# Optimization experiments

Hardware: AMD Instinct MI355X
Metric: run time of the kernel (lower is better)

The kernel has to match this reference:

```python
import jax, jax.numpy as jnp
import numpy as np

B, S, H = 32, 4096, 512

def setup_inputs() -> dict:
    key = jax.random.key(0)
    k1, k2, k3 = jax.random.split(key, 3)
    h_t = jax.random.normal(k1, (B, H), dtype=jnp.float32)
    context = jax.random.normal(k2, (B, S, H), dtype=jnp.float32)
    W = jax.random.normal(k3, (H, H), dtype=jnp.float32) * (1.0 / np.sqrt(H))
    pos = 7  # current cyclic-buffer write index (self.it % seq_len)
    return {"h_t": h_t, "context": context, "W": W, "pos": pos}

def reference(h_t, context, W, pos):
    # Luong 'general' attention: score[b,s] = h_t[b] . (W @ context[b,s])
    scores = jnp.einsum('bh,hk,bsk->bs', h_t, W, context)  # [B,S]
    attn = jax.nn.softmax(scores, axis=-1)                  # softmax over buffer slots
    # weighted sum over the context buffer -> [B,H]
    cntx = jnp.einsum('bs,bsh->bh', attn, context)
    # cyclic buffer write: add_vector(h_t) at slot pos (detached in original)
    new_buffer = context.at[:, pos % context.shape[1], :].set(h_t)
    return cntx, new_buffer
```

## Files before the change

### kernel.cpp

```cpp
#include <hip/hip_runtime.h>
#include <math.h>

constexpr int B = 32, S = 4096, H = 512;
constexpr int BDIM = 256;
constexpr int MAX_SPLIT = 64;

typedef float f4 __attribute__((ext_vector_type(4)));

__global__ __launch_bounds__(BDIM) void u_kernel(const float* __restrict__ h_t,
                                                 const float* __restrict__ W,
                                                 float* __restrict__ u) {
    const int b = blockIdx.y;
    const int k = blockIdx.x * BDIM + threadIdx.x;
    __shared__ float hs[H];
    for (int i = threadIdx.x; i < H; i += BDIM) hs[i] = h_t[b * H + i];
    __syncthreads();
    float acc = 0.f;
#pragma unroll 8
    for (int h = 0; h < H; ++h) acc = fmaf(hs[h], W[h * H + k], acc);
    u[b * H + k] = acc;
}

__global__ __launch_bounds__(BDIM) void flash_kernel(const float* __restrict__ ctx,
                                                     const float* __restrict__ h_t,
                                                     const float* __restrict__ u,
                                                     const int* __restrict__ posp,
                                                     float* __restrict__ newbuf,
                                                     float* __restrict__ pacc,
                                                     float* __restrict__ pml,
                                                     int nsplit) {
    const int b     = blockIdx.y;
    const int split = blockIdx.x;
    const int w     = threadIdx.x >> 6;
    const int lane  = threadIdx.x & 63;
    const int rpb   = S / nsplit;
    const int s0    = split * rpb;
    int pos = posp[0] % S; if (pos < 0) pos += S;

    const f4* ub = (const f4*)(u + (size_t)b * H);
    const f4 u0 = ub[lane], u1 = ub[64 + lane];
    const f4* hb = (const f4*)(h_t + (size_t)b * H);
    const f4 h0 = hb[lane], h1 = hb[64 + lane];

    float m = -INFINITY, l = 0.f;
    f4 a0 = {0.f, 0.f, 0.f, 0.f}, a1 = {0.f, 0.f, 0.f, 0.f};

#pragma unroll 2
    for (int s = s0 + w; s < s0 + rpb; s += 4) {
        const f4* crow = (const f4*)(ctx + ((size_t)b * S + s) * H);
        const f4 c0 = __builtin_nontemporal_load(crow + lane);
        const f4 c1 = __builtin_nontemporal_load(crow + 64 + lane);

        f4* orow = (f4*)(newbuf + ((size_t)b * S + s) * H);
        const f4 o0 = (s == pos) ? h0 : c0;
        const f4 o1 = (s == pos) ? h1 : c1;
        __builtin_nontemporal_store(o0, orow + lane);
        __builtin_nontemporal_store(o1, orow + 64 + lane);

        float d = c0.x * u0.x + c0.y * u0.y + c0.z * u0.z + c0.w * u0.w
                + c1.x * u1.x + c1.y * u1.y + c1.z * u1.z + c1.w * u1.w;
#pragma unroll
        for (int off = 32; off >= 1; off >>= 1) d += __shfl_xor(d, off);

        const float nm = fmaxf(m, d);
        const float sc = __expf(m - nm);
        const float p  = __expf(d - nm);
        a0 = a0 * sc + p * c0;
        a1 = a1 * sc + p * c1;
        l = l * sc + p;
        m = nm;
    }

    __shared__ float lacc[4][H];
    __shared__ float lml[4][2];
    f4* dst = (f4*)&lacc[w][0];
    dst[lane] = a0; dst[64 + lane] = a1;
    if (lane == 0) { lml[w][0] = m; lml[w][1] = l; }
    __syncthreads();

    const float m0 = lml[0][0], m1 = lml[1][0], m2 = lml[2][0], m3 = lml[3][0];
    const float M  = fmaxf(fmaxf(m0, m1), fmaxf(m2, m3));
    const float e0 = __expf(m0 - M), e1 = __expf(m1 - M);
    const float e2 = __expf(m2 - M), e3 = __expf(m3 - M);

    const int t    = threadIdx.x;
    const int pidx = b * nsplit + split;
    const float ca = e0 * lacc[0][t]       + e1 * lacc[1][t]
                   + e2 * lacc[2][t]       + e3 * lacc[3][t];
    const float cb = e0 * lacc[0][256 + t] + e1 * lacc[1][256 + t]
                   + e2 * lacc[2][256 + t] + e3 * lacc[3][256 + t];
    pacc[(size_t)pidx * H + t]       = ca;
    pacc[(size_t)pidx * H + 256 + t] = cb;
    if (t == 0) {
        const float L = e0 * lml[0][1] + e1 * lml[1][1]
                      + e2 * lml[2][1] + e3 * lml[3][1];
        pml[2 * pidx] = M; pml[2 * pidx + 1] = L;
    }
}

__global__ __launch_bounds__(BDIM) void combine_kernel(const float* __restrict__ pacc,
                                                       const float* __restrict__ pml,
                                                       float* __restrict__ cntx,
                                                       int nsplit) {
    const int b    = blockIdx.x;
    const int half = blockIdx.y;
    const int t    = threadIdx.x;
    const int col  = half * 256 + t;

    __shared__ float lm[MAX_SPLIT], ll[MAX_SPLIT];
    for (int p = t; p < nsplit; p += BDIM) {
        lm[p] = pml[2 * (b * nsplit + p)];
        ll[p] = pml[2 * (b * nsplit + p) + 1];
    }
    __syncthreads();

    float M = -INFINITY;
    for (int p = 0; p < nsplit; ++p) M = fmaxf(M, lm[p]);

    float acc = 0.f, L = 0.f;
    for (int p = 0; p < nsplit; ++p) {
        const float e = __expf(lm[p] - M);
        L   = fmaf(e, ll[p], L);
        acc = fmaf(e, pacc[(size_t)(b * nsplit + p) * H + col], acc);
    }
    cntx[b * H + col] = acc / L;
}

extern "C" void kernel_launch(void* const* d_in, const int* in_sizes, int n_in,
                              void* d_out, int out_size, void* d_ws, size_t ws_size,
                              hipStream_t stream) {
    const float* h_t = (const float*)d_in[0];
    const float* ctx = (const float*)d_in[1];
    const float* W   = (const float*)d_in[2];
    const int*   pos = (const int*)d_in[3];

    float* out    = (float*)d_out;
    float* cntx   = out;
    float* newbuf = out + (size_t)B * H;

    char*  ws = (char*)d_ws;
    float* u  = (float*)ws;
    const size_t u_bytes = (size_t)B * H * sizeof(float);

    int nsplit = MAX_SPLIT;
    while (nsplit > 1) {
        const size_t need = u_bytes
                          + (size_t)B * nsplit * H * sizeof(float)
                          + (size_t)B * nsplit * 2 * sizeof(float);
        if (need <= ws_size) break;
        nsplit >>= 1;
    }
    float* pacc = (float*)(ws + u_bytes);
    float* pml  = pacc + (size_t)B * nsplit * H;

    u_kernel<<<dim3(H / BDIM, B), BDIM, 0, stream>>>(h_t, W, u);
    flash_kernel<<<dim3(nsplit, B), BDIM, 0, stream>>>(ctx, h_t, u, pos, newbuf,
                                                       pacc, pml, nsplit);
    combine_kernel<<<dim3(B, 2), BDIM, 0, stream>>>(pacc, pml, cntx, nsplit);
}
```

Measured before the change: 131.3 us.

## Fuse combine into flash kernel via last-block atomic, use exp2 with lazy rescale

Removes the separate combine kernel launch: each split block increments a per-batch atomic counter, and the last block to finish merges all partial results. The counter is reset inside u_kernel. Scores are pre-scaled by log2(e) so exp2f can be used, and the running-max rescale is skipped unless the score exceeds the current max by a threshold, which cuts per-row exponentials. The u_kernel also gets four independent accumulators, and the flash loop unroll goes from 2 to 4. The costs are threadfence/atomic synchronisation and a serial tail combine done by one block per batch.

```diff
diff --git a/kernel.cpp b/kernel.cpp
--- a/kernel.cpp
+++ b/kernel.cpp
@@ -4,21 +4,30 @@
 constexpr int B = 32, S = 4096, H = 512;
 constexpr int BDIM = 256;
 constexpr int MAX_SPLIT = 64;
+constexpr float LOG2E = 1.44269504088896340736f;
+constexpr float DEFER_THR = 11.5415603f;
 
 typedef float f4 __attribute__((ext_vector_type(4)));
 
 __global__ __launch_bounds__(BDIM) void u_kernel(const float* __restrict__ h_t,
                                                  const float* __restrict__ W,
-                                                 float* __restrict__ u) {
+                                                 float* __restrict__ u,
+                                                 int* __restrict__ cnt) {
     const int b = blockIdx.y;
     const int k = blockIdx.x * BDIM + threadIdx.x;
+    if (blockIdx.x == 0 && b == 0 && threadIdx.x < B) cnt[threadIdx.x] = 0;
     __shared__ float hs[H];
     for (int i = threadIdx.x; i < H; i += BDIM) hs[i] = h_t[b * H + i];
     __syncthreads();
-    float acc = 0.f;
+    float a0 = 0.f, a1 = 0.f, a2 = 0.f, a3 = 0.f;
 #pragma unroll 8
-    for (int h = 0; h < H; ++h) acc = fmaf(hs[h], W[h * H + k], acc);
-    u[b * H + k] = acc;
+    for (int h = 0; h < H; h += 4) {
+        a0 = fmaf(hs[h],     W[(size_t)(h)     * H + k], a0);
+        a1 = fmaf(hs[h + 1], W[(size_t)(h + 1) * H + k], a1);
+        a2 = fmaf(hs[h + 2], W[(size_t)(h + 2) * H + k], a2);
+        a3 = fmaf(hs[h + 3], W[(size_t)(h + 3) * H + k], a3);
+    }
+    u[b * H + k] = ((a0 + a1) + (a2 + a3)) * LOG2E;
 }
 
 __global__ __launch_bounds__(BDIM) void flash_kernel(const float* __restrict__ ctx,
@@ -28,6 +37,8 @@
                                                      float* __restrict__ newbuf,
                                                      float* __restrict__ pacc,
                                                      float* __restrict__ pml,
+                                                     int* __restrict__ cnt,
+                                                     float* __restrict__ cntx,
                                                      int nsplit) {
     const int b     = blockIdx.y;
     const int split = blockIdx.x;
@@ -45,7 +56,7 @@
     float m = -INFINITY, l = 0.f;
     f4 a0 = {0.f, 0.f, 0.f, 0.f}, a1 = {0.f, 0.f, 0.f, 0.f};
 
-#pragma unroll 2
+#pragma unroll 4
     for (int s = s0 + w; s < s0 + rpb; s += 4) {
         const f4* crow = (const f4*)(ctx + ((size_t)b * S + s) * H);
         const f4 c0 = __builtin_nontemporal_load(crow + lane);
@@ -62,13 +73,14 @@
 #pragma unroll
         for (int off = 32; off >= 1; off >>= 1) d += __shfl_xor(d, off);
 
-        const float nm = fmaxf(m, d);
-        const float sc = __expf(m - nm);
-        const float p  = __expf(d - nm);
-        a0 = a0 * sc + p * c0;
-        a1 = a1 * sc + p * c1;
-        l = l * sc + p;
-        m = nm;
+        if (d > m + DEFER_THR) {
+            const float sc = exp2f(m - d);
+            a0 *= sc; a1 *= sc; l *= sc; m = d;
+        }
+        const float p = exp2f(d - m);
+        a0 += p * c0;
+        a1 += p * c1;
+        l  += p;
     }
 
     __shared__ float lacc[4][H];
@@ -80,8 +92,8 @@
 
     const float m0 = lml[0][0], m1 = lml[1][0], m2 = lml[2][0], m3 = lml[3][0];
     const float M  = fmaxf(fmaxf(m0, m1), fmaxf(m2, m3));
-    const float e0 = __expf(m0 - M), e1 = __expf(m1 - M);
-    const float e2 = __expf(m2 - M), e3 = __expf(m3 - M);
+    const float e0 = exp2f(m0 - M), e1 = exp2f(m1 - M);
+    const float e2 = exp2f(m2 - M), e3 = exp2f(m3 - M);
 
     const int t    = threadIdx.x;
     const int pidx = b * nsplit + split;
@@ -96,34 +108,33 @@
                       + e2 * lml[2][1] + e3 * lml[3][1];
         pml[2 * pidx] = M; pml[2 * pidx + 1] = L;
     }
-}
 
-__global__ __launch_bounds__(BDIM) void combine_kernel(const float* __restrict__ pacc,
-                                                       const float* __restrict__ pml,
-                                                       float* __restrict__ cntx,
-                                                       int nsplit) {
-    const int b    = blockIdx.x;
-    const int half = blockIdx.y;
-    const int t    = threadIdx.x;
-    const int col  = half * 256 + t;
+    __threadfence();
+    __syncthreads();
+    __shared__ int lastf;
+    if (t == 0) lastf = (atomicAdd(&cnt[b], 1) == nsplit - 1);
+    __syncthreads();
+    if (!lastf) return;
+    __threadfence();
 
-    __shared__ float lm[MAX_SPLIT], ll[MAX_SPLIT];
-    for (int p = t; p < nsplit; p += BDIM) {
-        lm[p] = pml[2 * (b * nsplit + p)];
-        ll[p] = pml[2 * (b * nsplit + p) + 1];
+    __shared__ float fm[MAX_SPLIT], fl[MAX_SPLIT];
+    if (t < nsplit) {
+        fm[t] = pml[2 * (b * nsplit + t)];
+        fl[t] = pml[2 * (b * nsplit + t) + 1];
     }
     __syncthreads();
-
-    float M = -INFINITY;
-    for (int p = 0; p < nsplit; ++p) M = fmaxf(M, lm[p]);
-
-    float acc = 0.f, L = 0.f;
+    float Mg = -INFINITY;
+    for (int p = 0; p < nsplit; ++p) Mg = fmaxf(Mg, fm[p]);
+    float L = 0.f, x0 = 0.f, x1 = 0.f;
+#pragma unroll 4
     for (int p = 0; p < nsplit; ++p) {
-        const float e = __expf(lm[p] - M);
-        L   = fmaf(e, ll[p], L);
-        acc = fmaf(e, pacc[(size_t)(b * nsplit + p) * H + col], acc);
+        const float e = exp2f(fm[p] - Mg);
+        L  = fmaf(e, fl[p], L);
+        x0 = fmaf(e, pacc[(size_t)(b * nsplit + p) * H + t],       x0);
+        x1 = fmaf(e, pacc[(size_t)(b * nsplit + p) * H + 256 + t], x1);
     }
-    cntx[b * H + col] = acc / L;
+    cntx[b * H + t]       = x0 / L;
+    cntx[b * H + 256 + t] = x1 / L;
 }
 
 extern "C" void kernel_launch(void* const* d_in, const int* in_sizes, int n_in,
@@ -146,15 +157,16 @@
     while (nsplit > 1) {
         const size_t need = u_bytes
                           + (size_t)B * nsplit * H * sizeof(float)
-                          + (size_t)B * nsplit * 2 * sizeof(float);
+                          + (size_t)B * nsplit * 2 * sizeof(float)
+                          + (size_t)B * sizeof(int);
         if (need <= ws_size) break;
         nsplit >>= 1;
     }
     float* pacc = (float*)(ws + u_bytes);
     float* pml  = pacc + (size_t)B * nsplit * H;
+    int*   cnt  = (int*)(pml + (size_t)B * nsplit * 2);
 
-    u_kernel<<<dim3(H / BDIM, B), BDIM, 0, stream>>>(h_t, W, u);
+    u_kernel<<<dim3(H / BDIM, B), BDIM, 0, stream>>>(h_t, W, u, cnt);
     flash_kernel<<<dim3(nsplit, B), BDIM, 0, stream>>>(ctx, h_t, u, pos, newbuf,
-                                                       pacc, pml, nsplit);
-    combine_kernel<<<dim3(B, 2), BDIM, 0, stream>>>(pacc, pml, cntx, nsplit);
+                                                       pacc, pml, cnt, cntx, nsplit);
 }
```

Result: slower. 524.1 us (+299.3%).

## Use log2-domain online softmax with lazy rescaling and regular context loads

Applied to the files above, without the earlier changes.

Pre-scales u by log2(e) so every exponential becomes exp2, and switches the online softmax to lazy rescaling: the running max is updated only when a new score exceeds it by a threshold, which drops the per-row rescale exp and multiplies. It also replaces nontemporal context loads with normal loads, raises the unroll factor of the flash loop, splits the u_kernel reduction across four accumulators, and unrolls the combine loop. Lazy rescaling lets exponentials grow up to 2^11.5 before renormalising, which trades a little overflow headroom for fewer operations. Normal loads may change cache behaviour on a streaming read of the large context tensor.

```diff
diff --git a/kernel.cpp b/kernel.cpp
--- a/kernel.cpp
+++ b/kernel.cpp
@@ -4,6 +4,8 @@
 constexpr int B = 32, S = 4096, H = 512;
 constexpr int BDIM = 256;
 constexpr int MAX_SPLIT = 64;
+constexpr float LOG2E = 1.44269504088896340736f;
+constexpr float DEFER_THR = 11.5415603f;
 
 typedef float f4 __attribute__((ext_vector_type(4)));
 
@@ -15,10 +17,15 @@
     __shared__ float hs[H];
     for (int i = threadIdx.x; i < H; i += BDIM) hs[i] = h_t[b * H + i];
     __syncthreads();
-    float acc = 0.f;
+    float a0 = 0.f, a1 = 0.f, a2 = 0.f, a3 = 0.f;
 #pragma unroll 8
-    for (int h = 0; h < H; ++h) acc = fmaf(hs[h], W[h * H + k], acc);
-    u[b * H + k] = acc;
+    for (int h = 0; h < H; h += 4) {
+        a0 = fmaf(hs[h],     W[(size_t)(h)     * H + k], a0);
+        a1 = fmaf(hs[h + 1], W[(size_t)(h + 1) * H + k], a1);
+        a2 = fmaf(hs[h + 2], W[(size_t)(h + 2) * H + k], a2);
+        a3 = fmaf(hs[h + 3], W[(size_t)(h + 3) * H + k], a3);
+    }
+    u[b * H + k] = ((a0 + a1) + (a2 + a3)) * LOG2E;
 }
 
 __global__ __launch_bounds__(BDIM) void flash_kernel(const float* __restrict__ ctx,
@@ -45,11 +52,11 @@
     float m = -INFINITY, l = 0.f;
     f4 a0 = {0.f, 0.f, 0.f, 0.f}, a1 = {0.f, 0.f, 0.f, 0.f};
 
-#pragma unroll 2
+#pragma unroll 4
     for (int s = s0 + w; s < s0 + rpb; s += 4) {
         const f4* crow = (const f4*)(ctx + ((size_t)b * S + s) * H);
-        const f4 c0 = __builtin_nontemporal_load(crow + lane);
-        const f4 c1 = __builtin_nontemporal_load(crow + 64 + lane);
+        const f4 c0 = crow[lane];
+        const f4 c1 = crow[64 + lane];
 
         f4* orow = (f4*)(newbuf + ((size_t)b * S + s) * H);
         const f4 o0 = (s == pos) ? h0 : c0;
@@ -62,13 +69,14 @@
 #pragma unroll
         for (int off = 32; off >= 1; off >>= 1) d += __shfl_xor(d, off);
 
-        const float nm = fmaxf(m, d);
-        const float sc = __expf(m - nm);
-        const float p  = __expf(d - nm);
-        a0 = a0 * sc + p * c0;
-        a1 = a1 * sc + p * c1;
-        l = l * sc + p;
-        m = nm;
+        if (d > m + DEFER_THR) {
+            const float sc = exp2f(m - d);
+            a0 *= sc; a1 *= sc; l *= sc; m = d;
+        }
+        const float p = exp2f(d - m);
+        a0 += p * c0;
+        a1 += p * c1;
+        l  += p;
     }
 
     __shared__ float lacc[4][H];
@@ -80,8 +88,8 @@
 
     const float m0 = lml[0][0], m1 = lml[1][0], m2 = lml[2][0], m3 = lml[3][0];
     const float M  = fmaxf(fmaxf(m0, m1), fmaxf(m2, m3));
-    const float e0 = __expf(m0 - M), e1 = __expf(m1 - M);
-    const float e2 = __expf(m2 - M), e3 = __expf(m3 - M);
+    const float e0 = exp2f(m0 - M), e1 = exp2f(m1 - M);
+    const float e2 = exp2f(m2 - M), e3 = exp2f(m3 - M);
 
     const int t    = threadIdx.x;
     const int pidx = b * nsplit + split;
@@ -118,8 +126,9 @@
     for (int p = 0; p < nsplit; ++p) M = fmaxf(M, lm[p]);
 
     float acc = 0.f, L = 0.f;
+#pragma unroll 4
     for (int p = 0; p < nsplit; ++p) {
-        const float e = __expf(lm[p] - M);
+        const float e = exp2f(lm[p] - M);
         L   = fmaf(e, ll[p], L);
         acc = fmaf(e, pacc[(size_t)(b * nsplit + p) * H + col], acc);
     }
```

Result: faster. 122.6 us (-6.6%).
